# Kernel tuning notes

Measured on AMD Instinct MI355X. Metric: run time of the kernel, lower is better.

The kernel has to match this reference:

```python
import jax, jax.numpy as jnp
import numpy as np

B, I, O, H = 1024, 128, 128, 5  # batch, input_size, output_size, hidden_size


def setup_inputs() -> dict:
    key = jax.random.key(0)
    ks = jax.random.split(key, 7)
    s = 0.3  # modest init scale, like torch default Linear init range
    return {
        "x": jax.random.normal(ks[0], (B, I), dtype=jnp.float32),
        # stacked per-edge MLP params: one tiny MLP per (output_node, input_node) edge
        "W1": jax.random.normal(ks[1], (O, I, H), dtype=jnp.float32) * s,  # Linear(1,H).weight
        "B1": jax.random.normal(ks[2], (O, I, H), dtype=jnp.float32) * s,
        "W2": jax.random.normal(ks[3], (O, I, H, H), dtype=jnp.float32) * s,  # Linear(H,H).weight (out,in)
        "B2": jax.random.normal(ks[4], (O, I, H), dtype=jnp.float32) * s,
        "W3": jax.random.normal(ks[5], (O, I, H), dtype=jnp.float32) * s,  # Linear(H,1).weight
        "B3": jax.random.normal(ks[6], (O, I), dtype=jnp.float32) * s,
    }


def reference(x, W1, B1, W2, B2, W3, B3):
    # Per-edge MLP, vectorized over all O*I edges at once.
    lrelu = lambda t: jax.nn.leaky_relu(t, negative_slope=0.01)  # torch LeakyReLU default
    # layer 1: scalar input -> H. [B,O,I,H]
    h1 = lrelu(x[:, None, :, None] * W1 + B1)
    # layer 2: H -> H per edge. torch Linear: y = h @ W.T, W is (out,in) -> contract 'in' axis
    h2 = lrelu(jnp.einsum("boih,oikh->boik", h1, W2) + B2)
    # layer 3: H -> scalar per edge, then sum over input nodes j
    y_edge = jnp.einsum("boih,oih->boi", h2, W3) + B3  # [B,O,I]
    return y_edge.sum(axis=2)  # [B,O]
```

## Files before the change

kernel.cpp:

```cpp
#include <hip/hip_runtime.h>
#include <hip/hip_fp16.h>

#define Bsz 1024
#define Isz 128
#define Osz 128
#define Hsz 5
#define GB 32
#define NG (Bsz / GB)

typedef _Float16 h2 __attribute__((ext_vector_type(2)));

__device__ __forceinline__ h2 lrelu2(h2 v) {
    return __builtin_elementwise_max(v, (h2)((_Float16)0.01f) * v);
}
__device__ __forceinline__ h2 splat2(float f) {
    const _Float16 h = (_Float16)f;
    h2 r; r.x = h; r.y = h; return r;
}

template <int CTRL>
__device__ __forceinline__ float dpp_add(float s) {
    int t = __builtin_amdgcn_update_dpp(0, __builtin_bit_cast(int, s),
                                        CTRL, 0xf, 0xf, true);
    return s + __builtin_bit_cast(float, t);
}
__device__ __forceinline__ float wave_sum64_lane63(float s) {
    s = dpp_add<0xB1>(s);
    s = dpp_add<0x4E>(s);
    s = dpp_add<0x141>(s);
    s = dpp_add<0x140>(s);
    s = dpp_add<0x142>(s);
    s = dpp_add<0x143>(s);
    return s;
}

__global__ __launch_bounds__(256, 6)
void kan_kernel(const float* __restrict__ x,
                const float* __restrict__ W1, const float* __restrict__ B1,
                const float* __restrict__ W2, const float* __restrict__ B2,
                const float* __restrict__ W3, const float* __restrict__ B3,
                float* __restrict__ out) {
    __shared__ float xs[GB * Isz];
    __shared__ float partial[4 * GB];

    const int tid = threadIdx.x;
    const int ob  = blockIdx.x & 63;
    const int g   = blockIdx.x >> 6;
    const int b0  = g * GB;
    const int w   = tid >> 6;
    const int l   = tid & 63;
    const int o   = 2 * ob + (w >> 1);
    const int i   = 64 * (w & 1) + l;
    const int e   = o * Isz + i;

    {
        const float4* xg = (const float4*)(x + (size_t)b0 * Isz);
        float4* xs4 = (float4*)xs;
        #pragma unroll
        for (int j = 0; j < (GB * Isz / 4) / 256; ++j)
            xs4[tid + 256 * j] = xg[tid + 256 * j];
    }

    h2 w1h[Hsz], b1h[Hsz], w2h[Hsz * Hsz], b2h[Hsz], w3h[Hsz];
    #pragma unroll
    for (int h = 0; h < Hsz; ++h) {
        w1h[h] = splat2(W1[(size_t)e * Hsz + h]);
        b1h[h] = splat2(B1[(size_t)e * Hsz + h]);
        b2h[h] = splat2(B2[(size_t)e * Hsz + h]);
        w3h[h] = splat2(W3[(size_t)e * Hsz + h]);
    }
    #pragma unroll
    for (int j = 0; j < Hsz * Hsz; ++j)
        w2h[j] = splat2(W2[(size_t)e * Hsz * Hsz + j]);

    const float s3w = wave_sum64_lane63(B3[e]);
    const float s3  = __builtin_bit_cast(float,
        __builtin_amdgcn_readlane(__builtin_bit_cast(int, s3w), 63));

    __syncthreads();

    float res = 0.0f;

    #pragma unroll
    for (int bl = 0; bl < GB; bl += 4) {
        float yv[4];
        #pragma unroll
        for (int u = 0; u < 2; ++u) {
            const int bb = bl + 2 * u;
            h2 a;
            a.x = (_Float16)xs[(bb + 0) * Isz + i];
            a.y = (_Float16)xs[(bb + 1) * Isz + i];

            h2 h1[Hsz];
            #pragma unroll
            for (int h = 0; h < Hsz; ++h)
                h1[h] = lrelu2(__builtin_elementwise_fma(a, w1h[h], b1h[h]));

            h2 yy = (h2)(_Float16)0.0f;
            #pragma unroll
            for (int k = 0; k < Hsz; ++k) {
                h2 s = b2h[k];
                #pragma unroll
                for (int h = 0; h < Hsz; ++h)
                    s = __builtin_elementwise_fma(h1[h], w2h[k * Hsz + h], s);
                s = lrelu2(s);
                yy = __builtin_elementwise_fma(s, w3h[k], yy);
            }
            yv[2 * u + 0] = (float)yy.x;
            yv[2 * u + 1] = (float)yy.y;
        }

        #pragma unroll
        for (int c = 0; c < 4; ++c) {
            const float s = wave_sum64_lane63(yv[c]);
            const float tot = __builtin_bit_cast(float,
                __builtin_amdgcn_readlane(__builtin_bit_cast(int, s), 63));
            if (l == bl + c) res = tot;
        }
    }

    if (l < GB) partial[w * GB + l] = res + s3;
    __syncthreads();

    if (tid < 2 * GB) {
        const int bl = tid & (GB - 1);
        const int oo = tid >> 5;
        const float v = partial[(2 * oo) * GB + bl] + partial[(2 * oo + 1) * GB + bl];
        out[(size_t)(b0 + bl) * Osz + (2 * ob + oo)] = v;
    }
}

extern "C" void kernel_launch(void* const* d_in, const int* in_sizes, int n_in,
                              void* d_out, int out_size, void* d_ws, size_t ws_size,
                              hipStream_t stream) {
    const float* x  = (const float*)d_in[0];
    const float* W1 = (const float*)d_in[1];
    const float* B1 = (const float*)d_in[2];
    const float* W2 = (const float*)d_in[3];
    const float* B2 = (const float*)d_in[4];
    const float* W3 = (const float*)d_in[5];
    const float* B3 = (const float*)d_in[6];
    float* out = (float*)d_out;

    const dim3 grid((Osz / 2) * NG);
    kan_kernel<<<grid, dim3(256), 0, stream>>>(x, W1, B1, W2, B2, W3, B3, out);
}
```

Baseline: 86.95 us.

## Pre-pack x as fp16 pairs in LDS and shorten wave reductions

The x tile is now converted to fp16 once during staging and stored as interleaved half2 pairs, so the inner loop does one 32-bit LDS load per pair instead of two float loads and two conversions. Each batch sample's cross-lane reduction now stops at 16-lane row sums instead of doing the full 64-lane DPP plus readlane. The four row partials per wave go to shared memory and are summed in the final epilogue. This removes the row_bcast steps and readlanes from the hot loop, in exchange for more shared-memory writes and a longer final summation.

```diff
diff --git a/kernel.cpp b/kernel.cpp
--- a/kernel.cpp
+++ b/kernel.cpp
@@ -24,11 +24,15 @@
                                         CTRL, 0xf, 0xf, true);
     return s + __builtin_bit_cast(float, t);
 }
-__device__ __forceinline__ float wave_sum64_lane63(float s) {
+__device__ __forceinline__ float wave_sum16_all(float s) {
     s = dpp_add<0xB1>(s);
     s = dpp_add<0x4E>(s);
     s = dpp_add<0x141>(s);
     s = dpp_add<0x140>(s);
+    return s;
+}
+__device__ __forceinline__ float wave_sum64_lane63(float s) {
+    s = wave_sum16_all(s);
     s = dpp_add<0x142>(s);
     s = dpp_add<0x143>(s);
     return s;
@@ -40,8 +44,9 @@
                 const float* __restrict__ W2, const float* __restrict__ B2,
                 const float* __restrict__ W3, const float* __restrict__ B3,
                 float* __restrict__ out) {
-    __shared__ float xs[GB * Isz];
-    __shared__ float partial[4 * GB];
+    __shared__ __align__(16) float xsh[GB / 2][Isz];
+    __shared__ float part2[4][4][GB];
+    __shared__ float s3s[4];
 
     const int tid = threadIdx.x;
     const int ob  = blockIdx.x & 63;
@@ -54,11 +59,26 @@
     const int e   = o * Isz + i;
 
     {
-        const float4* xg = (const float4*)(x + (size_t)b0 * Isz);
-        float4* xs4 = (float4*)xs;
+        const float* xg = x + (size_t)b0 * Isz;
         #pragma unroll
-        for (int j = 0; j < (GB * Isz / 4) / 256; ++j)
-            xs4[tid + 256 * j] = xg[tid + 256 * j];
+        for (int j = 0; j < 2; ++j) {
+            const int g2 = tid + 256 * j;
+            const int r  = g2 >> 5;
+            const int c  = 4 * (g2 & 31);
+            const float4 A = *(const float4*)(xg + (size_t)(2 * r) * Isz + c);
+            const float4 Bv = *(const float4*)(xg + (size_t)(2 * r + 1) * Isz + c);
+            h2 v0, v1, v2, v3;
+            v0.x = (_Float16)A.x;  v0.y = (_Float16)Bv.x;
+            v1.x = (_Float16)A.y;  v1.y = (_Float16)Bv.y;
+            v2.x = (_Float16)A.z;  v2.y = (_Float16)Bv.z;
+            v3.x = (_Float16)A.w;  v3.y = (_Float16)Bv.w;
+            float4 wv;
+            wv.x = __builtin_bit_cast(float, v0);
+            wv.y = __builtin_bit_cast(float, v1);
+            wv.z = __builtin_bit_cast(float, v2);
+            wv.w = __builtin_bit_cast(float, v3);
+            *(float4*)&xsh[r][c] = wv;
+        }
     }
 
     h2 w1h[Hsz], b1h[Hsz], w2h[Hsz * Hsz], b2h[Hsz], w3h[Hsz];
@@ -73,23 +93,21 @@
     for (int j = 0; j < Hsz * Hsz; ++j)
         w2h[j] = splat2(W2[(size_t)e * Hsz * Hsz + j]);
 
-    const float s3w = wave_sum64_lane63(B3[e]);
-    const float s3  = __builtin_bit_cast(float,
-        __builtin_amdgcn_readlane(__builtin_bit_cast(int, s3w), 63));
+    {
+        const float s3w = wave_sum64_lane63(B3[e]);
+        const float s3  = __builtin_bit_cast(float,
+            __builtin_amdgcn_readlane(__builtin_bit_cast(int, s3w), 63));
+        if (l == 0) s3s[w] = s3;
+    }
 
     __syncthreads();
-
-    float res = 0.0f;
 
     #pragma unroll
     for (int bl = 0; bl < GB; bl += 4) {
         float yv[4];
         #pragma unroll
         for (int u = 0; u < 2; ++u) {
-            const int bb = bl + 2 * u;
-            h2 a;
-            a.x = (_Float16)xs[(bb + 0) * Isz + i];
-            a.y = (_Float16)xs[(bb + 1) * Isz + i];
+            const h2 a = __builtin_bit_cast(h2, xsh[(bl >> 1) + u][i]);
 
             h2 h1[Hsz];
             #pragma unroll
@@ -110,22 +128,29 @@
             yv[2 * u + 1] = (float)yy.y;
         }
 
-        #pragma unroll
-        for (int c = 0; c < 4; ++c) {
-            const float s = wave_sum64_lane63(yv[c]);
-            const float tot = __builtin_bit_cast(float,
-                __builtin_amdgcn_readlane(__builtin_bit_cast(int, s), 63));
-            if (l == bl + c) res = tot;
-        }
+        const float g0 = wave_sum16_all(yv[0]);
+        const float g1 = wave_sum16_all(yv[1]);
+        const float g2 = wave_sum16_all(yv[2]);
+        const float g3 = wave_sum16_all(yv[3]);
+
+        const float s01 = (l & 1) ? g1 : g0;
+        const float s23 = (l & 1) ? g3 : g2;
+        const float val = (l & 2) ? s23 : s01;
+        if ((l & 15) < 4)
+            part2[w][l >> 4][bl + (l & 3)] = val;
     }
 
-    if (l < GB) partial[w * GB + l] = res + s3;
     __syncthreads();
 
     if (tid < 2 * GB) {
         const int bl = tid & (GB - 1);
         const int oo = tid >> 5;
-        const float v = partial[(2 * oo) * GB + bl] + partial[(2 * oo + 1) * GB + bl];
+        float v = s3s[2 * oo] + s3s[2 * oo + 1];
+        #pragma unroll
+        for (int ww = 0; ww < 2; ++ww)
+            #pragma unroll
+            for (int gg = 0; gg < 4; ++gg)
+                v += part2[2 * oo + ww][gg][bl];
         out[(size_t)(b0 + bl) * Osz + (2 * ob + oo)] = v;
     }
 }
```

Result: slower. 92.53 us (+6.4%).
